# Performance work log

Measured on AMD Instinct MI355X. Metric: run time of the kernel, lower is better.

## Reference

```python
import jax, jax.numpy as jnp
import numpy as np

EPS = 1e-5
NEG_INF = -1e38


def q_shift(x, H, W, gamma=0.25, s=1):
    # x: (B, T, C) with T = H*W. Four channel groups shifted by 1 pixel in +W,-W,+H,-H.
    B, T, C = x.shape
    g = int(C * gamma)
    x4 = x.reshape(B, H, W, C)
    o0 = jnp.pad(x4[..., 0:g], ((0, 0), (0, 0), (s, 0), (0, 0)))[:, :, :W, :]      # shift right along W
    o1 = jnp.pad(x4[..., g:2 * g], ((0, 0), (0, 0), (0, s), (0, 0)))[:, :, s:, :]  # shift left along W
    o2 = jnp.pad(x4[..., 2 * g:3 * g], ((0, 0), (s, 0), (0, 0), (0, 0)))[:, :H, :, :]  # shift down along H
    o3 = jnp.pad(x4[..., 3 * g:4 * g], ((0, 0), (0, s), (0, 0), (0, 0)))[:, s:, :, :]  # shift up along H
    parts = [o0, o1, o2, o3]
    if 4 * g < C:
        parts.append(jnp.zeros((B, H, W, C - 4 * g), x.dtype))
    return jnp.concatenate(parts, axis=-1).reshape(B, T, C)


def wkv(w, u, k, v):
    # Numerically-stable RWKV WKV recurrence.
    # w,u: (C,); k,v: (B,T,C) -> y: (B,T,C)
    B, T, C = k.shape

    def step(carry, kv):
        a, b, p = carry
        kt, vt = kv
        ww = u + kt
        p2 = jnp.maximum(p, ww)
        e1 = jnp.exp(p - p2)
        e2 = jnp.exp(ww - p2)
        y = (e1 * a + e2 * vt) / (e1 * b + e2)
        ww2 = p + w
        p3 = jnp.maximum(ww2, kt)
        f1 = jnp.exp(ww2 - p3)
        f2 = jnp.exp(kt - p3)
        return (f1 * a + f2 * vt, f1 * b + f2, p3), y

    init = (jnp.zeros((B, C), k.dtype), jnp.zeros((B, C), k.dtype),
            jnp.full((B, C), NEG_INF, k.dtype))
    kT = jnp.swapaxes(k, 0, 1)
    vT = jnp.swapaxes(v, 0, 1)
    _, ys = jax.lax.scan(step, init, (kT, vT))
    return jnp.swapaxes(ys, 0, 1)


def layer_norm(x, g, b):
    m = jnp.mean(x, axis=-1, keepdims=True)
    v = jnp.mean(jnp.square(x - m), axis=-1, keepdims=True)
    return (x - m) * jax.lax.rsqrt(v + EPS) * g + b


def setup_inputs() -> dict:
    key = jax.random.key(0)
    ks = jax.random.split(key, 16)
    B, H, W, C = 8, 64, 64, 768
    T = H * W
    sc = 1.0 / np.sqrt(C)
    inp = {
        "x": jax.random.normal(ks[0], (B, T, C), jnp.float32),
        "spatial_decay": jax.random.normal(ks[1], (C,), jnp.float32) * 0.1,
        "spatial_first": jax.random.normal(ks[2], (C,), jnp.float32) * 0.1,
        "mix_k": jax.random.uniform(ks[3], (1, 1, C), jnp.float32),
        "mix_v": jax.random.uniform(ks[4], (1, 1, C), jnp.float32),
        "mix_r": jax.random.uniform(ks[5], (1, 1, C), jnp.float32),
        "Wk": jax.random.normal(ks[6], (C, C), jnp.float32) * sc,
        "Wv": jax.random.normal(ks[7], (C, C), jnp.float32) * sc,
        "Wr": jax.random.normal(ks[8], (C, C), jnp.float32) * sc,
        "Wo": jax.random.normal(ks[9], (C, C), jnp.float32) * sc,
        "ln_g": jnp.ones((C,), jnp.float32),
        "ln_b": jnp.zeros((C,), jnp.float32),
        "Wd1": jax.random.normal(ks[10], (C, C // 4), jnp.float32) * sc,
        "bd1": jnp.zeros((C // 4,), jnp.float32),
        "Wd2": jax.random.normal(ks[11], (C // 4, C), jnp.float32) * (2.0 / np.sqrt(C)),
        "bd2": jnp.full((C,), -3.0, jnp.float32),
        "H": H,
        "W": W,
    }
    return inp


def reference(x, spatial_decay, spatial_first, mix_k, mix_v, mix_r,
              Wk, Wv, Wr, Wo, ln_g, ln_b, Wd1, bd1, Wd2, bd2, H, W):
    B, T, C = x.shape
    xx = q_shift(x, H, W)
    xk = x * mix_k + xx * (1.0 - mix_k)
    xv = x * mix_v + xx * (1.0 - mix_v)
    xr = x * mix_r + xx * (1.0 - mix_r)
    k = xk @ Wk
    v = xv @ Wv
    sr = jax.nn.sigmoid(xr @ Wr)
    # frequency-adaptive decay modulation from global context
    gctx = jnp.mean(x, axis=1)                       # (B, C)
    h = jnp.tanh(gctx @ Wd1 + bd1)                   # (B, C/4)
    mod = jax.nn.sigmoid(h @ Wd2 + bd2)              # (B, C)
    w = spatial_decay + jnp.mean(mod, axis=0)        # (C,)
    y = wkv(w, spatial_first, k, v)                  # (B, T, C)
    y = layer_norm(y, ln_g, ln_b)
    return (sr * y) @ Wo
```

## Files before the change

kernel.cpp:

```cpp
#include <hip/hip_runtime.h>
#include <hip/hip_bf16.h>

typedef __hip_bfloat16 bf16;
typedef short short8 __attribute__((ext_vector_type(8)));
typedef float f32x4 __attribute__((ext_vector_type(4)));

#define T_SEQ 4096
#define HH 64
#define WW2 64
#define C_DIM 768
#define CQ 192
#define LCH 32
#define NCH (T_SEQ / LCH)
#define NCG (C_DIM / 8)

__device__ __forceinline__ float b2f(bf16 h) { return __bfloat162float(h); }
__device__ __forceinline__ bf16 f2b(float f) { return __float2bfloat16(f); }
__device__ __forceinline__ float sigmoid_stable(float m) {
  float e = __expf(-fabsf(m));
  return (m >= 0.f) ? 1.f / (1.f + e) : e / (1.f + e);
}

union V16 { uint4 u; bf16 h[8]; };

__global__ void k_detect(const unsigned* __restrict__ p, int* __restrict__ flag) {
  if (threadIdx.x == 0 && blockIdx.x == 0)
    *flag = ((p[0] & 0xFFFFu) == 0u) ? 1 : 0;
}

__global__ void k_convert_b(const void* __restrict__ src, bf16* __restrict__ dst,
                            int n, const int* __restrict__ flag) {
  int i = blockIdx.x * blockDim.x + threadIdx.x;
  if (i >= n) return;
  dst[i] = (*flag) ? f2b(((const float*)src)[i]) : ((const bf16*)src)[i];
}

__global__ void k_convert_f(const void* __restrict__ src, float* __restrict__ dst,
                            int n, const int* __restrict__ flag) {
  int i = blockIdx.x * blockDim.x + threadIdx.x;
  if (i >= n) return;
  dst[i] = (*flag) ? ((const float*)src)[i] : b2f(((const bf16*)src)[i]);
}

__global__ void k_transpose_d(const void* __restrict__ src, bf16* __restrict__ dst,
                              const int* __restrict__ flag) {
  __shared__ bf16 tile[32][33];
  bool f32 = (*flag != 0);
  int bx = blockIdx.x * 32, by = blockIdx.y * 32;
  int tx = threadIdx.x, ty = threadIdx.y;
  for (int j = ty; j < 32; j += 8) {
    size_t idx = (size_t)(by + j) * C_DIM + bx + tx;
    tile[j][tx] = f32 ? f2b(((const float*)src)[idx]) : ((const bf16*)src)[idx];
  }
  __syncthreads();
  for (int j = ty; j < 32; j += 8)
    dst[(size_t)(bx + j) * C_DIM + by + tx] = tile[tx][j];
}

__global__ void k_shift_mix1(const void* __restrict__ xsrc,
                             const float* __restrict__ mix,
                             bf16* __restrict__ dst, int BT,
                             const int* __restrict__ flag) {
  int idx = blockIdx.x * blockDim.x + threadIdx.x;
  if (idx >= BT * (C_DIM / 8)) return;
  bool f32 = (*flag != 0);
  int c8 = (idx % (C_DIM / 8)) * 8;
  int tg = idx / (C_DIM / 8);
  int t = tg & (T_SEQ - 1);
  int hh = t >> 6, ww = t & (WW2 - 1);
  int g = c8 / CQ;
  int d; bool valid;
  if (g == 0)      { valid = (ww >= 1);        d = -1;   }
  else if (g == 1) { valid = (ww <= WW2 - 2);  d = 1;    }
  else if (g == 2) { valid = (hh >= 1);        d = -WW2; }
  else             { valid = (hh <= HH - 2);   d = WW2;  }
  ptrdiff_t base = (ptrdiff_t)tg * C_DIM + c8;
  float fx[8], fxx[8];
  if (f32) {
    const float* xp = (const float*)xsrc;
#pragma unroll
    for (int i = 0; i < 8; i++) fx[i] = xp[base + i];
    if (valid) {
#pragma unroll
      for (int i = 0; i < 8; i++) fxx[i] = xp[base + (ptrdiff_t)d * C_DIM + i];
    } else {
#pragma unroll
      for (int i = 0; i < 8; i++) fxx[i] = 0.f;
    }
  } else {
    const bf16* xp = (const bf16*)xsrc;
    V16 xin; xin.u = *(const uint4*)(xp + base);
    V16 xxv;
    if (valid) xxv.u = *(const uint4*)(xp + base + (ptrdiff_t)d * C_DIM);
    else       xxv.u = make_uint4(0u, 0u, 0u, 0u);
#pragma unroll
    for (int i = 0; i < 8; i++) { fx[i] = b2f(xin.h[i]); fxx[i] = b2f(xxv.h[i]); }
  }
  V16 o;
#pragma unroll
  for (int i = 0; i < 8; i++)
    o.h[i] = f2b(fxx[i] + mix[c8 + i] * (fx[i] - fxx[i]));
  *(uint4*)(dst + base) = o.u;
}

__global__ void k_gctx(const void* __restrict__ xsrc, float* __restrict__ gctx,
                       const int* __restrict__ flag) {
  bool f32 = (*flag != 0);
  int c = threadIdx.x;
  int chunk = blockIdx.x;
  int b = blockIdx.y;
  size_t base = ((size_t)b * T_SEQ + (size_t)chunk * 128) * C_DIM + c;
  float s = 0.f;
  if (f32) {
    const float* p = (const float*)xsrc;
    for (int t = 0; t < 128; t++) s += p[base + (size_t)t * C_DIM];
  } else {
    const bf16* p = (const bf16*)xsrc;
    for (int t = 0; t < 128; t++) s += b2f(p[base + (size_t)t * C_DIM]);
  }
  atomicAdd(&gctx[b * C_DIM + c], s);
}

__global__ void k_mod(const float* __restrict__ gctx,
                      const bf16* __restrict__ Wd1, const float* __restrict__ bd1,
                      const bf16* __restrict__ Wd2, const float* __restrict__ bd2,
                      float* __restrict__ wsum, int B) {
  __shared__ float hsh[CQ];
  int b = blockIdx.x, j = threadIdx.x;
  const float invT = 1.0f / (float)T_SEQ;
  float acc = bd1[j];
  for (int i = 0; i < C_DIM; i++)
    acc += (gctx[b * C_DIM + i] * invT) * b2f(Wd1[(size_t)i * CQ + j]);
  hsh[j] = tanhf(acc);
  __syncthreads();
  float invB = 1.0f / (float)B;
  for (int cc = j; cc < C_DIM; cc += CQ) {
    float m = bd2[cc];
    for (int jj = 0; jj < CQ; jj++)
      m += hsh[jj] * b2f(Wd2[(size_t)jj * C_DIM + cc]);
    atomicAdd(&wsum[cc], sigmoid_stable(m) * invB);
  }
}

__device__ __forceinline__ void g2l16(const void* g, void* s) {
  __builtin_amdgcn_global_load_lds(
      (const __attribute__((address_space(1))) unsigned int*)g,
      (__attribute__((address_space(3))) unsigned int*)s, 16, 0, 0);
}

template <int MODE>
__global__ __launch_bounds__(256) void k_gemm_bt(const bf16* __restrict__ A,
                                                 const bf16* __restrict__ Bt,
                                                 void* __restrict__ Cout,
                                                 const int* __restrict__ flag) {
  const int K = C_DIM, N = C_DIM;
  __shared__ bf16 sA[128 * 32];
  __shared__ bf16 sB[128 * 32];
  int tid = threadIdx.x;
  int wv = tid >> 6, lane = tid & 63;
  int lm = lane & 15, quad = lane >> 4;
  int m0 = blockIdx.x * 128, n0 = blockIdx.y * 128;
  int wm = (wv & 1) * 64, wn = (wv >> 1) * 64;
  bool f32out = (MODE == 2) && (*flag != 0);

  f32x4 acc[4][4];
#pragma unroll
  for (int i = 0; i < 4; i++)
#pragma unroll
    for (int j = 0; j < 4; j++) acc[i][j] = f32x4{0.f, 0.f, 0.f, 0.f};

  const bf16* Abase = A + (size_t)m0 * K;
  const bf16* Bbase = Bt + (size_t)n0 * K;
  int ci0 = wv * 128 + lane;
  int ci1 = wv * 128 + 64 + lane;

  for (int kc = 0; kc < K; kc += 32) {
    g2l16(Abase + (size_t)(ci0 >> 2) * K + kc + (ci0 & 3) * 8, (char*)sA + (size_t)(wv * 128) * 16);
    g2l16(Abase + (size_t)(ci1 >> 2) * K + kc + (ci1 & 3) * 8, (char*)sA + (size_t)(wv * 128 + 64) * 16);
    g2l16(Bbase + (size_t)(ci0 >> 2) * K + kc + (ci0 & 3) * 8, (char*)sB + (size_t)(wv * 128) * 16);
    g2l16(Bbase + (size_t)(ci1 >> 2) * K + kc + (ci1 & 3) * 8, (char*)sB + (size_t)(wv * 128 + 64) * 16);
    __syncthreads();
    short8 af[4], bfr[4];
#pragma unroll
    for (int i = 0; i < 4; i++)
      af[i] = *(const short8*)(sA + (size_t)(wm + i * 16 + lm) * 32 + quad * 8);
#pragma unroll
    for (int j = 0; j < 4; j++)
      bfr[j] = *(const short8*)(sB + (size_t)(wn + j * 16 + lm) * 32 + quad * 8);
#pragma unroll
    for (int i = 0; i < 4; i++)
#pragma unroll
      for (int j = 0; j < 4; j++)
        acc[i][j] = __builtin_amdgcn_mfma_f32_16x16x32_bf16(af[i], bfr[j], acc[i][j], 0, 0, 0);
    __syncthreads();
  }
#pragma unroll
  for (int i = 0; i < 4; i++)
#pragma unroll
    for (int j = 0; j < 4; j++)
#pragma unroll
      for (int r = 0; r < 4; r++) {
        int m = wm + i * 16 + quad * 4 + r;
        int n = wn + j * 16 + lm;
        float v = acc[i][j][r];
        if (MODE == 1) v = sigmoid_stable(v);
        size_t oidx = (size_t)(m0 + m) * N + n0 + n;
        if (MODE == 2) {
          if (f32out) ((float*)Cout)[oidx] = v;
          else        ((bf16*)Cout)[oidx] = f2b(v);
        } else {
          ((bf16*)Cout)[oidx] = f2b(v);
        }
      }
}


__global__ __launch_bounds__(256) void k_wkv_p1(
    const bf16* __restrict__ kb, const bf16* __restrict__ vb,
    const float* __restrict__ sd, const float* __restrict__ wsum,
    float* __restrict__ ca, float* __restrict__ cb, float* __restrict__ cp, int B) {
  int gid = blockIdx.x * 256 + threadIdx.x;
  if (gid >= B * NCH * NCG) return;
  int cg = gid % NCG;
  int ch = (gid / NCG) % NCH;
  int b  = gid / (NCG * NCH);
  int c0 = cg * 8;
  float w[8], a[8], bb[8], p[8];
#pragma unroll
  for (int i = 0; i < 8; i++) {
    w[i] = sd[c0 + i] + wsum[c0 + i];
    a[i] = 0.f; bb[i] = 0.f; p[i] = -1e38f;
  }
  const bf16* kp = kb + ((size_t)b * T_SEQ + (size_t)ch * LCH) * C_DIM + c0;
  const bf16* vp = vb + ((size_t)b * T_SEQ + (size_t)ch * LCH) * C_DIM + c0;
  V16 kv, vv, kn, vn;
  kv.u = *(const uint4*)kp;
  vv.u = *(const uint4*)vp;
  kn = kv; vn = vv;
  for (int t = 0; t < LCH; t++) {
    if (t + 1 < LCH) {
      kn.u = *(const uint4*)(kp + (size_t)(t + 1) * C_DIM);
      vn.u = *(const uint4*)(vp + (size_t)(t + 1) * C_DIM);
    }
#pragma unroll
    for (int i = 0; i < 8; i++) {
      float kt = b2f(kv.h[i]), vt = b2f(vv.h[i]);
      float ww2 = p[i] + w[i];
      float p3 = fmaxf(ww2, kt);
      float f1 = __expf(ww2 - p3);
      float f2 = __expf(kt - p3);
      a[i] = f1 * a[i] + f2 * vt;
      bb[i] = f1 * bb[i] + f2;
      p[i] = p3;
    }
    kv = kn; vv = vn;
  }
  size_t so = ((size_t)b * NCH + ch) * C_DIM + c0;
#pragma unroll
  for (int i = 0; i < 8; i++) { ca[so + i] = a[i]; cb[so + i] = bb[i]; cp[so + i] = p[i]; }
}

__global__ void k_wkv_p2(float* __restrict__ ca, float* __restrict__ cb,
                         float* __restrict__ cp,
                         const float* __restrict__ sd, const float* __restrict__ wsum,
                         int B) {
  int tid = blockIdx.x * blockDim.x + threadIdx.x;
  if (tid >= B * C_DIM) return;
  int b = tid / C_DIM, c = tid % C_DIM;
  float wL = (sd[c] + wsum[c]) * (float)LCH;
  float a = 0.f, bb = 0.f, p = -1e38f;
  for (int base = 0; base < NCH; base += 16) {
    float la[16], lb[16], lp[16];
#pragma unroll
    for (int j = 0; j < 16; j++) {
      size_t idx = ((size_t)b * NCH + base + j) * C_DIM + c;
      la[j] = ca[idx]; lb[j] = cb[idx]; lp[j] = cp[idx];
    }
#pragma unroll
    for (int j = 0; j < 16; j++) {
      size_t idx = ((size_t)b * NCH + base + j) * C_DIM + c;
      ca[idx] = a; cb[idx] = bb; cp[idx] = p;
      float pw = p + wL;
      float pn = fmaxf(pw, lp[j]);
      float e1 = __expf(pw - pn);
      float e2 = __expf(lp[j] - pn);
      a = e1 * a + e2 * la[j];
      bb = e1 * bb + e2 * lb[j];
      p = pn;
    }
  }
}

__global__ __launch_bounds__(256) void k_wkv_p3(
    const bf16* __restrict__ kb, const bf16* __restrict__ vb,
    const float* __restrict__ sd, const float* __restrict__ sf,
    const float* __restrict__ wsum,
    const float* __restrict__ ca, const float* __restrict__ cb,
    const float* __restrict__ cp, bf16* __restrict__ y, int B) {
  int gid = blockIdx.x * 256 + threadIdx.x;
  if (gid >= B * NCH * NCG) return;
  int cg = gid % NCG;
  int ch = (gid / NCG) % NCH;
  int b  = gid / (NCG * NCH);
  int c0 = cg * 8;
  size_t so = ((size_t)b * NCH + ch) * C_DIM + c0;
  float w[8], u[8], aa[8], bb[8], pp[8];
#pragma unroll
  for (int i = 0; i < 8; i++) {
    w[i] = sd[c0 + i] + wsum[c0 + i];
    u[i] = sf[c0 + i];
    aa[i] = ca[so + i]; bb[i] = cb[so + i]; pp[i] = cp[so + i];
  }
  const bf16* kp = kb + ((size_t)b * T_SEQ + (size_t)ch * LCH) * C_DIM + c0;
  const bf16* vp = vb + ((size_t)b * T_SEQ + (size_t)ch * LCH) * C_DIM + c0;
  bf16* yp = y + ((size_t)b * T_SEQ + (size_t)ch * LCH) * C_DIM + c0;
  V16 kv, vv, kn, vn;
  kv.u = *(const uint4*)kp;
  vv.u = *(const uint4*)vp;
  kn = kv; vn = vv;
  for (int t = 0; t < LCH; t++) {
    if (t + 1 < LCH) {
      kn.u = *(const uint4*)(kp + (size_t)(t + 1) * C_DIM);
      vn.u = *(const uint4*)(vp + (size_t)(t + 1) * C_DIM);
    }
    V16 o;
#pragma unroll
    for (int i = 0; i < 8; i++) {
      float kt = b2f(kv.h[i]), vt = b2f(vv.h[i]);
      float ww = u[i] + kt;
      float p2 = fmaxf(pp[i], ww);
      float e1 = __expf(pp[i] - p2);
      float e2 = __expf(ww - p2);
      o.h[i] = f2b((e1 * aa[i] + e2 * vt) / (e1 * bb[i] + e2));
      float ww2 = pp[i] + w[i];
      float p3 = fmaxf(ww2, kt);
      float f1 = __expf(ww2 - p3);
      float f2 = __expf(kt - p3);
      aa[i] = f1 * aa[i] + f2 * vt;
      bb[i] = f1 * bb[i] + f2;
      pp[i] = p3;
    }
    *(uint4*)(yp + (size_t)t * C_DIM) = o.u;
    kv = kn; vv = vn;
  }
}

__global__ __launch_bounds__(256) void k_ln_mul(const bf16* __restrict__ y,
                                                const bf16* __restrict__ sr,
                                                const float* __restrict__ lng,
                                                const float* __restrict__ lnb,
                                                bf16* __restrict__ out) {
  int row = blockIdx.x;
  int tid = threadIdx.x;
  const bf16* yr = y + (size_t)row * C_DIM;
  float v0 = b2f(yr[tid]), v1 = b2f(yr[tid + 256]), v2 = b2f(yr[tid + 512]);
  float s1 = v0 + v1 + v2;
  float s2 = v0 * v0 + v1 * v1 + v2 * v2;
#pragma unroll
  for (int off = 32; off >= 1; off >>= 1) {
    s1 += __shfl_xor(s1, off, 64);
    s2 += __shfl_xor(s2, off, 64);
  }
  __shared__ float sh1[4], sh2[4];
  int wv = tid >> 6, lane = tid & 63;
  if (lane == 0) { sh1[wv] = s1; sh2[wv] = s2; }
  __syncthreads();
  float t1 = sh1[0] + sh1[1] + sh1[2] + sh1[3];
  float t2 = sh2[0] + sh2[1] + sh2[2] + sh2[3];
  float mean = t1 * (1.f / (float)C_DIM);
  float var = t2 * (1.f / (float)C_DIM) - mean * mean;
  float rstd = rsqrtf(var + 1e-5f);
  const bf16* srr = sr + (size_t)row * C_DIM;
  bf16* orow = out + (size_t)row * C_DIM;
  float vv[3] = {v0, v1, v2};
#pragma unroll
  for (int kk = 0; kk < 3; kk++) {
    int c = tid + kk * 256;
    float r = (vv[kk] - mean) * rstd * lng[c] + lnb[c];
    orow[c] = f2b(r * b2f(srr[c]));
  }
}

extern "C" void kernel_launch(void* const* d_in, const int* in_sizes, int n_in,
                              void* d_out, int out_size, void* d_ws, size_t ws_size,
                              hipStream_t stream) {
  const void* x   = d_in[0];
  const void* sd  = d_in[1];
  const void* sf  = d_in[2];
  const void* mk  = d_in[3];
  const void* mv  = d_in[4];
  const void* mr  = d_in[5];
  const void* Wk  = d_in[6];
  const void* Wv  = d_in[7];
  const void* Wr  = d_in[8];
  const void* Wo  = d_in[9];
  const void* lng = d_in[10];
  const void* lnb = d_in[11];
  const void* Wd1 = d_in[12];
  const void* bd1 = d_in[13];
  const void* Wd2 = d_in[14];
  const void* bd2 = d_in[15];

  const int C = in_sizes[1];
  const int BT = in_sizes[0] / C;
  const int B = BT / T_SEQ;

  char* ws = (char*)d_ws;
  const size_t S = (size_t)BT * C * sizeof(bf16);
  const size_t WB = (size_t)C * C * sizeof(bf16);
  const size_t WD = (size_t)C * CQ * sizeof(bf16);
  bf16* slot0 = (bf16*)(ws + 0 * S);
  bf16* slot1 = (bf16*)(ws + 1 * S);
  char* p = ws + 2 * S;
  bf16* WkT = (bf16*)p; p += WB;
  bf16* WvT = (bf16*)p; p += WB;
  bf16* WrT = (bf16*)p; p += WB;
  bf16* WoT = (bf16*)p; p += WB;
  bf16* Wd1c = (bf16*)p; p += WD;
  bf16* Wd2c = (bf16*)p; p += WD;
  float* sd_f  = (float*)p; p += C * 4;
  float* sf_f  = (float*)p; p += C * 4;
  float* mk_f  = (float*)p; p += C * 4;
  float* mv_f  = (float*)p; p += C * 4;
  float* mr_f  = (float*)p; p += C * 4;
  float* lng_f = (float*)p; p += C * 4;
  float* lnb_f = (float*)p; p += C * 4;
  float* bd2_f = (float*)p; p += C * 4;
  float* bd1_f = (float*)p; p += CQ * 4;
  float* gctx  = (float*)p; p += (size_t)B * C * 4;
  float* wsum  = (float*)p; p += C * 4;
  int* flag    = (int*)p; p += 16;
  p = (char*)(((uintptr_t)p + 15) & ~(uintptr_t)15);
  float* ca = (float*)p; p += (size_t)B * NCH * C * 4;
  float* cb = (float*)p; p += (size_t)B * NCH * C * 4;
  float* cp = (float*)p; p += (size_t)B * NCH * C * 4;

  bf16* stage = (bf16*)d_out;

  k_detect<<<1, 64, 0, stream>>>((const unsigned*)lng, flag);
  hipMemsetAsync(gctx, 0, (size_t)(B * C + C) * sizeof(float), stream);

  k_convert_f<<<3, 256, 0, stream>>>(sd,  sd_f,  C, flag);
  k_convert_f<<<3, 256, 0, stream>>>(sf,  sf_f,  C, flag);
  k_convert_f<<<3, 256, 0, stream>>>(mk,  mk_f,  C, flag);
  k_convert_f<<<3, 256, 0, stream>>>(mv,  mv_f,  C, flag);
  k_convert_f<<<3, 256, 0, stream>>>(mr,  mr_f,  C, flag);
  k_convert_f<<<3, 256, 0, stream>>>(lng, lng_f, C, flag);
  k_convert_f<<<3, 256, 0, stream>>>(lnb, lnb_f, C, flag);
  k_convert_f<<<3, 256, 0, stream>>>(bd2, bd2_f, C, flag);
  k_convert_f<<<1, 256, 0, stream>>>(bd1, bd1_f, CQ, flag);
  k_convert_b<<<(C * CQ + 255) / 256, 256, 0, stream>>>(Wd1, Wd1c, C * CQ, flag);
  k_convert_b<<<(C * CQ + 255) / 256, 256, 0, stream>>>(Wd2, Wd2c, C * CQ, flag);

  dim3 tb(32, 8), tg(C / 32, C / 32);
  k_transpose_d<<<tg, tb, 0, stream>>>(Wk, WkT, flag);
  k_transpose_d<<<tg, tb, 0, stream>>>(Wv, WvT, flag);
  k_transpose_d<<<tg, tb, 0, stream>>>(Wr, WrT, flag);
  k_transpose_d<<<tg, tb, 0, stream>>>(Wo, WoT, flag);

  k_gctx<<<dim3(32, B), C, 0, stream>>>(x, gctx, flag);
  k_mod<<<B, CQ, 0, stream>>>(gctx, Wd1c, bd1_f, Wd2c, bd2_f, wsum, B);

  int nthr = BT * (C / 8);
  int nblk = (nthr + 255) / 256;
  dim3 gg(BT / 128, C / 128);

  k_shift_mix1<<<nblk, 256, 0, stream>>>(x, mk_f, stage, BT, flag);
  k_gemm_bt<0><<<gg, 256, 0, stream>>>(stage, WkT, slot0, flag);
  k_shift_mix1<<<nblk, 256, 0, stream>>>(x, mv_f, stage, BT, flag);
  k_gemm_bt<0><<<gg, 256, 0, stream>>>(stage, WvT, slot1, flag);

  int scan_threads = B * NCH * NCG;
  k_wkv_p1<<<(scan_threads + 255) / 256, 256, 0, stream>>>(slot0, slot1, sd_f, wsum, ca, cb, cp, B);
  k_wkv_p2<<<(B * C + 255) / 256, 256, 0, stream>>>(ca, cb, cp, sd_f, wsum, B);
  k_wkv_p3<<<(scan_threads + 255) / 256, 256, 0, stream>>>(slot0, slot1, sd_f, sf_f, wsum, ca, cb, cp, stage, B);

  k_shift_mix1<<<nblk, 256, 0, stream>>>(x, mr_f, slot0, BT, flag);
  k_gemm_bt<1><<<gg, 256, 0, stream>>>(slot0, WrT, slot1, flag);
  k_ln_mul<<<BT, 256, 0, stream>>>(stage, slot1, lng_f, lnb_f, slot0);
  k_gemm_bt<2><<<gg, 256, 0, stream>>>(slot0, WoT, d_out, flag);
}
```

Before: 716.4 us.

## Fuse shift-mix passes, fold LayerNorm into gemm epilogue, and stage stores via LDS

The three shift-mix passes are merged into one kernel that reads x once, writes xk/xv/xr, and also emits per-block partial sums for the global context, so the separate gctx pass goes away. The LayerNorm-multiply kernel is split into a row-stats kernel plus an epilogue in the Wr gemm that applies sigmoid, normalization and the multiply. Gemm output now goes through LDS for coalesced 16-byte stores, with a float path for f32 output. The grid is swapped so blocks along N are adjacent. The scan loops are unrolled four deep with prefetching, and the small parameter conversions are batched into one launch. The fused path needs an extra full-size workspace slot and falls back to the old order when the workspace is too small.

```diff
diff --git a/kernel.cpp b/kernel.cpp
--- a/kernel.cpp
+++ b/kernel.cpp
@@ -13,6 +13,7 @@
 #define LCH 32
 #define NCH (T_SEQ / LCH)
 #define NCG (C_DIM / 8)
+#define TCH 16
 
 __device__ __forceinline__ float b2f(bf16 h) { return __bfloat162float(h); }
 __device__ __forceinline__ bf16 f2b(float f) { return __float2bfloat16(f); }
@@ -35,11 +36,20 @@
   dst[i] = (*flag) ? f2b(((const float*)src)[i]) : ((const bf16*)src)[i];
 }
 
-__global__ void k_convert_f(const void* __restrict__ src, float* __restrict__ dst,
-                            int n, const int* __restrict__ flag) {
-  int i = blockIdx.x * blockDim.x + threadIdx.x;
-  if (i >= n) return;
-  dst[i] = (*flag) ? ((const float*)src)[i] : b2f(((const bf16*)src)[i]);
+__global__ void k_convert_small(
+    const void* s0, const void* s1, const void* s2, const void* s3, const void* s4,
+    const void* s5, const void* s6, const void* s7, const void* s8,
+    float* d0, float* d1, float* d2, float* d3, float* d4,
+    float* d5, float* d6, float* d7, float* d8, const int* __restrict__ flag) {
+  const void* srcs[9] = {s0, s1, s2, s3, s4, s5, s6, s7, s8};
+  float* dsts[9] = {d0, d1, d2, d3, d4, d5, d6, d7, d8};
+  int a = blockIdx.x;
+  int n = (a == 8) ? CQ : C_DIM;
+  const void* s = srcs[a];
+  float* d = dsts[a];
+  bool f32 = (*flag != 0);
+  for (int i = threadIdx.x; i < n; i += 256)
+    d[i] = f32 ? ((const float*)s)[i] : b2f(((const bf16*)s)[i]);
 }
 
 __global__ void k_transpose_d(const void* __restrict__ src, bf16* __restrict__ dst,
@@ -103,6 +113,93 @@
   *(uint4*)(dst + base) = o.u;
 }
 
+__global__ __launch_bounds__(256) void k_shift_mix3(
+    const void* __restrict__ xsrc,
+    const float* __restrict__ mk, const float* __restrict__ mv, const float* __restrict__ mr,
+    bf16* __restrict__ xk, bf16* __restrict__ xv, bf16* __restrict__ xr,
+    float* __restrict__ gpart, const int* __restrict__ flag) {
+  __shared__ float sh[C_DIM];
+  int tid = threadIdx.x;
+  sh[tid] = 0.f; sh[tid + 256] = 0.f; sh[tid + 512] = 0.f;
+  __syncthreads();
+  int gid = blockIdx.x * 256 + tid;
+  bool f32 = (*flag != 0);
+  int cg = gid % NCG;
+  int tc = gid / NCG;
+  int c0 = cg * 8;
+  int b = tc / (T_SEQ / TCH);
+  int t0 = (tc % (T_SEQ / TCH)) * TCH;
+  int g = c0 / CQ;
+  float mkv[8], mvv[8], mrv[8];
+#pragma unroll
+  for (int i = 0; i < 8; i++) { mkv[i] = mk[c0 + i]; mvv[i] = mv[c0 + i]; mrv[i] = mr[c0 + i]; }
+  float gs[8];
+#pragma unroll
+  for (int i = 0; i < 8; i++) gs[i] = 0.f;
+  for (int tt = 0; tt < TCH; tt++) {
+    int t = t0 + tt;
+    int hh = t >> 6, ww = t & (WW2 - 1);
+    int d; bool valid;
+    if (g == 0)      { valid = (ww >= 1);        d = -1;   }
+    else if (g == 1) { valid = (ww <= WW2 - 2);  d = 1;    }
+    else if (g == 2) { valid = (hh >= 1);        d = -WW2; }
+    else             { valid = (hh <= HH - 2);   d = WW2;  }
+    ptrdiff_t base = ((ptrdiff_t)b * T_SEQ + t) * C_DIM + c0;
+    float fx[8], fxx[8];
+    if (f32) {
+      const float* xp = (const float*)xsrc;
+      float4 a0 = *(const float4*)(xp + base);
+      float4 a1 = *(const float4*)(xp + base + 4);
+      fx[0] = a0.x; fx[1] = a0.y; fx[2] = a0.z; fx[3] = a0.w;
+      fx[4] = a1.x; fx[5] = a1.y; fx[6] = a1.z; fx[7] = a1.w;
+      if (valid) {
+        float4 b0 = *(const float4*)(xp + base + (ptrdiff_t)d * C_DIM);
+        float4 b1 = *(const float4*)(xp + base + (ptrdiff_t)d * C_DIM + 4);
+        fxx[0] = b0.x; fxx[1] = b0.y; fxx[2] = b0.z; fxx[3] = b0.w;
+        fxx[4] = b1.x; fxx[5] = b1.y; fxx[6] = b1.z; fxx[7] = b1.w;
+      } else {
+#pragma unroll
+        for (int i = 0; i < 8; i++) fxx[i] = 0.f;
+      }
+    } else {
+      const bf16* xp = (const bf16*)xsrc;
+      V16 xin; xin.u = *(const uint4*)(xp + base);
+      V16 xxv;
+      if (valid) xxv.u = *(const uint4*)(xp + base + (ptrdiff_t)d * C_DIM);
+      else       xxv.u = make_uint4(0u, 0u, 0u, 0u);
+#pragma unroll
+      for (int i = 0; i < 8; i++) { fx[i] = b2f(xin.h[i]); fxx[i] = b2f(xxv.h[i]); }
+    }
+    V16 ok, ov, orr;
+#pragma unroll
+    for (int i = 0; i < 8; i++) {
+      gs[i] += fx[i];
+      ok.h[i]  = f2b(fxx[i] + mkv[i] * (fx[i] - fxx[i]));
+      ov.h[i]  = f2b(fxx[i] + mvv[i] * (fx[i] - fxx[i]));
+      orr.h[i] = f2b(fxx[i] + mrv[i] * (fx[i] - fxx[i]));
+    }
+    *(uint4*)(xk + base) = ok.u;
+    *(uint4*)(xv + base) = ov.u;
+    *(uint4*)(xr + base) = orr.u;
+  }
+#pragma unroll
+  for (int i = 0; i < 8; i++) atomicAdd(&sh[c0 + i], gs[i]);
+  __syncthreads();
+  float* gp = gpart + (size_t)blockIdx.x * C_DIM;
+  gp[tid] = sh[tid]; gp[tid + 256] = sh[tid + 256]; gp[tid + 512] = sh[tid + 512];
+}
+
+__global__ void k_gctx_reduce(const float* __restrict__ gpart, float* __restrict__ gctx,
+                              int B, int blk_per_b) {
+  int idx = blockIdx.x * 256 + threadIdx.x;
+  if (idx >= B * C_DIM) return;
+  int b = idx / C_DIM, c = idx % C_DIM;
+  const float* pp = gpart + (size_t)b * blk_per_b * C_DIM + c;
+  float s = 0.f;
+  for (int j = 0; j < blk_per_b; j++) s += pp[(size_t)j * C_DIM];
+  gctx[idx] = s;
+}
+
 __global__ void k_gctx(const void* __restrict__ xsrc, float* __restrict__ gctx,
                        const int* __restrict__ flag) {
   bool f32 = (*flag != 0);
@@ -149,19 +246,20 @@
 }
 
 template <int MODE>
-__global__ __launch_bounds__(256) void k_gemm_bt(const bf16* __restrict__ A,
-                                                 const bf16* __restrict__ Bt,
-                                                 void* __restrict__ Cout,
-                                                 const int* __restrict__ flag) {
+__global__ __launch_bounds__(256) void k_gemm_bt(
+    const bf16* __restrict__ A, const bf16* __restrict__ Bt, void* __restrict__ Cout,
+    const bf16* __restrict__ Y, const float* __restrict__ stats,
+    const float* __restrict__ lng, const float* __restrict__ lnb,
+    const int* __restrict__ flag) {
   const int K = C_DIM, N = C_DIM;
-  __shared__ bf16 sA[128 * 32];
-  __shared__ bf16 sB[128 * 32];
+  __shared__ __align__(16) char smem[32768];
+  bf16* sA = (bf16*)smem;
+  bf16* sB = (bf16*)(smem + 8192);
   int tid = threadIdx.x;
   int wv = tid >> 6, lane = tid & 63;
   int lm = lane & 15, quad = lane >> 4;
-  int m0 = blockIdx.x * 128, n0 = blockIdx.y * 128;
+  int n0 = blockIdx.x * 128, m0 = blockIdx.y * 128;
   int wm = (wv & 1) * 64, wn = (wv >> 1) * 64;
-  bool f32out = (MODE == 2) && (*flag != 0);
 
   f32x4 acc[4][4];
 #pragma unroll
@@ -194,26 +292,107 @@
         acc[i][j] = __builtin_amdgcn_mfma_f32_16x16x32_bf16(af[i], bfr[j], acc[i][j], 0, 0, 0);
     __syncthreads();
   }
-#pragma unroll
-  for (int i = 0; i < 4; i++)
-#pragma unroll
-    for (int j = 0; j < 4; j++)
-#pragma unroll
-      for (int r = 0; r < 4; r++) {
-        int m = wm + i * 16 + quad * 4 + r;
-        int n = wn + j * 16 + lm;
-        float v = acc[i][j][r];
-        if (MODE == 1) v = sigmoid_stable(v);
-        size_t oidx = (size_t)(m0 + m) * N + n0 + n;
-        if (MODE == 2) {
-          if (f32out) ((float*)Cout)[oidx] = v;
-          else        ((bf16*)Cout)[oidx] = f2b(v);
-        } else {
-          ((bf16*)Cout)[oidx] = f2b(v);
+
+  bool f32out = (MODE == 2) && (*flag != 0);
+  if (!f32out) {
+    bf16* sC = (bf16*)smem;
+#pragma unroll
+    for (int i = 0; i < 4; i++)
+#pragma unroll
+      for (int j = 0; j < 4; j++)
+#pragma unroll
+        for (int r = 0; r < 4; r++) {
+          int m = wm + i * 16 + quad * 4 + r;
+          int n = wn + j * 16 + lm;
+          float v = acc[i][j][r];
+          if (MODE == 1 || MODE == 3) v = sigmoid_stable(v);
+          sC[m * 128 + n] = f2b(v);
         }
+    __syncthreads();
+    int c16 = tid & 15, r0 = tid >> 4;
+#pragma unroll
+    for (int it = 0; it < 8; it++) {
+      int r = r0 + it * 16;
+      V16 val; val.u = *(const uint4*)(sC + r * 128 + c16 * 8);
+      size_t gbase = (size_t)(m0 + r) * N + n0 + c16 * 8;
+      if (MODE == 3) {
+        float mu = stats[2 * (m0 + r)], rs = stats[2 * (m0 + r) + 1];
+        V16 yv; yv.u = *(const uint4*)(Y + gbase);
+        const float* lg = lng + n0 + c16 * 8;
+        const float* lb = lnb + n0 + c16 * 8;
+        V16 o;
+#pragma unroll
+        for (int jj = 0; jj < 8; jj++)
+          o.h[jj] = f2b(b2f(val.h[jj]) * ((b2f(yv.h[jj]) - mu) * rs * lg[jj] + lb[jj]));
+        *(uint4*)((bf16*)Cout + gbase) = o.u;
+      } else {
+        *(uint4*)((bf16*)Cout + gbase) = val.u;
       }
-}
-
+    }
+  } else {
+    float* sCf = (float*)smem;
+#pragma unroll
+    for (int half = 0; half < 2; half++) {
+      if (half) __syncthreads();
+      if ((wv & 1) == half) {
+#pragma unroll
+        for (int i = 0; i < 4; i++)
+#pragma unroll
+          for (int j = 0; j < 4; j++)
+#pragma unroll
+            for (int r = 0; r < 4; r++) {
+              int mrow = i * 16 + quad * 4 + r;
+              int n = wn + j * 16 + lm;
+              sCf[mrow * 128 + n] = acc[i][j][r];
+            }
+      }
+      __syncthreads();
+      int c32 = tid & 31, r0 = tid >> 5;
+#pragma unroll
+      for (int it = 0; it < 8; it++) {
+        int r = r0 + it * 8;
+        float4 val = *(const float4*)(sCf + r * 128 + c32 * 4);
+        *(float4*)((float*)Cout + (size_t)(m0 + half * 64 + r) * N + n0 + c32 * 4) = val;
+      }
+    }
+  }
+}
+
+__device__ __forceinline__ void wkv_acc_step(const V16& kv, const V16& vv,
+    const float* __restrict__ w, float* a, float* bb, float* p) {
+#pragma unroll
+  for (int i = 0; i < 8; i++) {
+    float kt = b2f(kv.h[i]), vt = b2f(vv.h[i]);
+    float ww2 = p[i] + w[i];
+    float p3 = fmaxf(ww2, kt);
+    float f1 = __expf(ww2 - p3);
+    float f2 = __expf(kt - p3);
+    a[i] = f1 * a[i] + f2 * vt;
+    bb[i] = f1 * bb[i] + f2;
+    p[i] = p3;
+  }
+}
+
+__device__ __forceinline__ void wkv_out_step(const V16& kv, const V16& vv,
+    const float* __restrict__ w, const float* __restrict__ u,
+    float* aa, float* bb, float* pp, V16& o) {
+#pragma unroll
+  for (int i = 0; i < 8; i++) {
+    float kt = b2f(kv.h[i]), vt = b2f(vv.h[i]);
+    float ww = u[i] + kt;
+    float p2 = fmaxf(pp[i], ww);
+    float e1 = __expf(pp[i] - p2);
+    float e2 = __expf(ww - p2);
+    o.h[i] = f2b((e1 * aa[i] + e2 * vt) / (e1 * bb[i] + e2));
+    float ww2 = pp[i] + w[i];
+    float p3 = fmaxf(ww2, kt);
+    float f1 = __expf(ww2 - p3);
+    float f2 = __expf(kt - p3);
+    aa[i] = f1 * aa[i] + f2 * vt;
+    bb[i] = f1 * bb[i] + f2;
+    pp[i] = p3;
+  }
+}
 
 __global__ __launch_bounds__(256) void k_wkv_p1(
     const bf16* __restrict__ kb, const bf16* __restrict__ vb,
@@ -225,39 +404,36 @@
   int ch = (gid / NCG) % NCH;
   int b  = gid / (NCG * NCH);
   int c0 = cg * 8;
-  float w[8], a[8], bb[8], p[8];
+  float w[8], a[8], bbv[8], p[8];
 #pragma unroll
   for (int i = 0; i < 8; i++) {
     w[i] = sd[c0 + i] + wsum[c0 + i];
-    a[i] = 0.f; bb[i] = 0.f; p[i] = -1e38f;
+    a[i] = 0.f; bbv[i] = 0.f; p[i] = -1e38f;
   }
   const bf16* kp = kb + ((size_t)b * T_SEQ + (size_t)ch * LCH) * C_DIM + c0;
   const bf16* vp = vb + ((size_t)b * T_SEQ + (size_t)ch * LCH) * C_DIM + c0;
-  V16 kv, vv, kn, vn;
-  kv.u = *(const uint4*)kp;
-  vv.u = *(const uint4*)vp;
-  kn = kv; vn = vv;
-  for (int t = 0; t < LCH; t++) {
-    if (t + 1 < LCH) {
-      kn.u = *(const uint4*)(kp + (size_t)(t + 1) * C_DIM);
-      vn.u = *(const uint4*)(vp + (size_t)(t + 1) * C_DIM);
-    }
-#pragma unroll
-    for (int i = 0; i < 8; i++) {
-      float kt = b2f(kv.h[i]), vt = b2f(vv.h[i]);
-      float ww2 = p[i] + w[i];
-      float p3 = fmaxf(ww2, kt);
-      float f1 = __expf(ww2 - p3);
-      float f2 = __expf(kt - p3);
-      a[i] = f1 * a[i] + f2 * vt;
-      bb[i] = f1 * bb[i] + f2;
-      p[i] = p3;
-    }
-    kv = kn; vv = vn;
-  }
+  V16 k0, k1, k2, k3, v0, v1, v2, v3;
+  k0.u = *(const uint4*)(kp);              v0.u = *(const uint4*)(vp);
+  k1.u = *(const uint4*)(kp + C_DIM);      v1.u = *(const uint4*)(vp + C_DIM);
+  k2.u = *(const uint4*)(kp + 2 * C_DIM);  v2.u = *(const uint4*)(vp + 2 * C_DIM);
+  k3.u = *(const uint4*)(kp + 3 * C_DIM);  v3.u = *(const uint4*)(vp + 3 * C_DIM);
+  for (int t = 0; t + 4 < LCH; t += 4) {
+    wkv_acc_step(k0, v0, w, a, bbv, p);
+    k0.u = *(const uint4*)(kp + (size_t)(t + 4) * C_DIM); v0.u = *(const uint4*)(vp + (size_t)(t + 4) * C_DIM);
+    wkv_acc_step(k1, v1, w, a, bbv, p);
+    k1.u = *(const uint4*)(kp + (size_t)(t + 5) * C_DIM); v1.u = *(const uint4*)(vp + (size_t)(t + 5) * C_DIM);
+    wkv_acc_step(k2, v2, w, a, bbv, p);
+    k2.u = *(const uint4*)(kp + (size_t)(t + 6) * C_DIM); v2.u = *(const uint4*)(vp + (size_t)(t + 6) * C_DIM);
+    wkv_acc_step(k3, v3, w, a, bbv, p);
+    k3.u = *(const uint4*)(kp + (size_t)(t + 7) * C_DIM); v3.u = *(const uint4*)(vp + (size_t)(t + 7) * C_DIM);
+  }
+  wkv_acc_step(k0, v0, w, a, bbv, p);
+  wkv_acc_step(k1, v1, w, a, bbv, p);
+  wkv_acc_step(k2, v2, w, a, bbv, p);
+  wkv_acc_step(k3, v3, w, a, bbv, p);
   size_t so = ((size_t)b * NCH + ch) * C_DIM + c0;
 #pragma unroll
-  for (int i = 0; i < 8; i++) { ca[so + i] = a[i]; cb[so + i] = bb[i]; cp[so + i] = p[i]; }
+  for (int i = 0; i < 8; i++) { ca[so + i] = a[i]; cb[so + i] = bbv[i]; cp[so + i] = p[i]; }
 }
 
 __global__ void k_wkv_p2(float* __restrict__ ca, float* __restrict__ cb,
@@ -304,52 +480,47 @@
   int b  = gid / (NCG * NCH);
   int c0 = cg * 8;
   size_t so = ((size_t)b * NCH + ch) * C_DIM + c0;
-  float w[8], u[8], aa[8], bb[8], pp[8];
+  float w[8], u[8], aa[8], bbv[8], pp[8];
 #pragma unroll
   for (int i = 0; i < 8; i++) {
     w[i] = sd[c0 + i] + wsum[c0 + i];
     u[i] = sf[c0 + i];
-    aa[i] = ca[so + i]; bb[i] = cb[so + i]; pp[i] = cp[so + i];
+    aa[i] = ca[so + i]; bbv[i] = cb[so + i]; pp[i] = cp[so + i];
   }
   const bf16* kp = kb + ((size_t)b * T_SEQ + (size_t)ch * LCH) * C_DIM + c0;
   const bf16* vp = vb + ((size_t)b * T_SEQ + (size_t)ch * LCH) * C_DIM + c0;
   bf16* yp = y + ((size_t)b * T_SEQ + (size_t)ch * LCH) * C_DIM + c0;
-  V16 kv, vv, kn, vn;
-  kv.u = *(const uint4*)kp;
-  vv.u = *(const uint4*)vp;
-  kn = kv; vn = vv;
-  for (int t = 0; t < LCH; t++) {
-    if (t + 1 < LCH) {
-      kn.u = *(const uint4*)(kp + (size_t)(t + 1) * C_DIM);
-      vn.u = *(const uint4*)(vp + (size_t)(t + 1) * C_DIM);
-    }
-    V16 o;
-#pragma unroll
-    for (int i = 0; i < 8; i++) {
-      float kt = b2f(kv.h[i]), vt = b2f(vv.h[i]);
-      float ww = u[i] + kt;
-      float p2 = fmaxf(pp[i], ww);
-      float e1 = __expf(pp[i] - p2);
-      float e2 = __expf(ww - p2);
-      o.h[i] = f2b((e1 * aa[i] + e2 * vt) / (e1 * bb[i] + e2));
-      float ww2 = pp[i] + w[i];
-      float p3 = fmaxf(ww2, kt);
-      float f1 = __expf(ww2 - p3);
-      float f2 = __expf(kt - p3);
-      aa[i] = f1 * aa[i] + f2 * vt;
-      bb[i] = f1 * bb[i] + f2;
-      pp[i] = p3;
-    }
+  V16 k0, k1, k2, k3, v0, v1, v2, v3, o;
+  k0.u = *(const uint4*)(kp);              v0.u = *(const uint4*)(vp);
+  k1.u = *(const uint4*)(kp + C_DIM);      v1.u = *(const uint4*)(vp + C_DIM);
+  k2.u = *(const uint4*)(kp + 2 * C_DIM);  v2.u = *(const uint4*)(vp + 2 * C_DIM);
+  k3.u = *(const uint4*)(kp + 3 * C_DIM);  v3.u = *(const uint4*)(vp + 3 * C_DIM);
+  for (int t = 0; t + 4 < LCH; t += 4) {
+    wkv_out_step(k0, v0, w, u, aa, bbv, pp, o);
     *(uint4*)(yp + (size_t)t * C_DIM) = o.u;
-    kv = kn; vv = vn;
-  }
-}
-
-__global__ __launch_bounds__(256) void k_ln_mul(const bf16* __restrict__ y,
-                                                const bf16* __restrict__ sr,
-                                                const float* __restrict__ lng,
-                                                const float* __restrict__ lnb,
-                                                bf16* __restrict__ out) {
+    k0.u = *(const uint4*)(kp + (size_t)(t + 4) * C_DIM); v0.u = *(const uint4*)(vp + (size_t)(t + 4) * C_DIM);
+    wkv_out_step(k1, v1, w, u, aa, bbv, pp, o);
+    *(uint4*)(yp + (size_t)(t + 1) * C_DIM) = o.u;
+    k1.u = *(const uint4*)(kp + (size_t)(t + 5) * C_DIM); v1.u = *(const uint4*)(vp + (size_t)(t + 5) * C_DIM);
+    wkv_out_step(k2, v2, w, u, aa, bbv, pp, o);
+    *(uint4*)(yp + (size_t)(t + 2) * C_DIM) = o.u;
+    k2.u = *(const uint4*)(kp + (size_t)(t + 6) * C_DIM); v2.u = *(const uint4*)(vp + (size_t)(t + 6) * C_DIM);
+    wkv_out_step(k3, v3, w, u, aa, bbv, pp, o);
+    *(uint4*)(yp + (size_t)(t + 3) * C_DIM) = o.u;
+    k3.u = *(const uint4*)(kp + (size_t)(t + 7) * C_DIM); v3.u = *(const uint4*)(vp + (size_t)(t + 7) * C_DIM);
+  }
+  wkv_out_step(k0, v0, w, u, aa, bbv, pp, o);
+  *(uint4*)(yp + (size_t)(LCH - 4) * C_DIM) = o.u;
+  wkv_out_step(k1, v1, w, u, aa, bbv, pp, o);
+  *(uint4*)(yp + (size_t)(LCH - 3) * C_DIM) = o.u;
+  wkv_out_step(k2, v2, w, u, aa, bbv, pp, o);
+  *(uint4*)(yp + (size_t)(LCH - 2) * C_DIM) = o.u;
+  wkv_out_step(k3, v3, w, u, aa, bbv, pp, o);
+  *(uint4*)(yp + (size_t)(LCH - 1) * C_DIM) = o.u;
+}
+
+__global__ __launch_bounds__(256) void k_ln_stats(const bf16* __restrict__ y,
+                                                  float* __restrict__ stats) {
   int row = blockIdx.x;
   int tid = threadIdx.x;
   const bf16* yr = y + (size_t)row * C_DIM;
@@ -365,19 +536,13 @@
   int wv = tid >> 6, lane = tid & 63;
   if (lane == 0) { sh1[wv] = s1; sh2[wv] = s2; }
   __syncthreads();
-  float t1 = sh1[0] + sh1[1] + sh1[2] + sh1[3];
-  float t2 = sh2[0] + sh2[1] + sh2[2] + sh2[3];
-  float mean = t1 * (1.f / (float)C_DIM);
-  float var = t2 * (1.f / (float)C_DIM) - mean * mean;
-  float rstd = rsqrtf(var + 1e-5f);
-  const bf16* srr = sr + (size_t)row * C_DIM;
-  bf16* orow = out + (size_t)row * C_DIM;
-  float vv[3] = {v0, v1, v2};
-#pragma unroll
-  for (int kk = 0; kk < 3; kk++) {
-    int c = tid + kk * 256;
-    float r = (vv[kk] - mean) * rstd * lng[c] + lnb[c];
-    orow[c] = f2b(r * b2f(srr[c]));
+  if (tid == 0) {
+    float t1 = sh1[0] + sh1[1] + sh1[2] + sh1[3];
+    float t2 = sh2[0] + sh2[1] + sh2[2] + sh2[3];
+    float mean = t1 * (1.f / (float)C_DIM);
+    float var = t2 * (1.f / (float)C_DIM) - mean * mean;
+    stats[2 * row] = mean;
+    stats[2 * row + 1] = rsqrtf(var + 1e-5f);
   }
 }
 
@@ -405,13 +570,22 @@
   const int BT = in_sizes[0] / C;
   const int B = BT / T_SEQ;
 
-  char* ws = (char*)d_ws;
-  const size_t S = (size_t)BT * C * sizeof(bf16);
+  const size_t S  = (size_t)BT * C * sizeof(bf16);
   const size_t WB = (size_t)C * C * sizeof(bf16);
   const size_t WD = (size_t)C * CQ * sizeof(bf16);
-  bf16* slot0 = (bf16*)(ws + 0 * S);
-  bf16* slot1 = (bf16*)(ws + 1 * S);
-  char* p = ws + 2 * S;
+  const size_t CS = (size_t)B * NCH * C * sizeof(float);
+  const int nblk_mix = (BT / TCH) * NCG / 256;
+  const int blk_per_b = nblk_mix / B;
+  const size_t GP = (size_t)nblk_mix * C * sizeof(float);
+  const size_t rest = 4 * WB + 2 * WD + ((size_t)8 * C + CQ + (size_t)B * C + C) * 4
+                      + 16 + 15 + 3 * CS + (size_t)BT * 8 + GP + 256;
+  const bool fused = (ws_size >= 3 * S + rest);
+
+  char* p = (char*)d_ws;
+  bf16* slot0 = (bf16*)p; p += S;
+  bf16* slot1 = (bf16*)p; p += S;
+  bf16* slot2 = nullptr;
+  if (fused) { slot2 = (bf16*)p; p += S; }
   bf16* WkT = (bf16*)p; p += WB;
   bf16* WvT = (bf16*)p; p += WB;
   bf16* WrT = (bf16*)p; p += WB;
@@ -431,24 +605,20 @@
   float* wsum  = (float*)p; p += C * 4;
   int* flag    = (int*)p; p += 16;
   p = (char*)(((uintptr_t)p + 15) & ~(uintptr_t)15);
-  float* ca = (float*)p; p += (size_t)B * NCH * C * 4;
-  float* cb = (float*)p; p += (size_t)B * NCH * C * 4;
-  float* cp = (float*)p; p += (size_t)B * NCH * C * 4;
+  float* ca = (float*)p; p += CS;
+  float* cb = (float*)p; p += CS;
+  float* cp = (float*)p; p += CS;
+  float* stats = (float*)p; p += (size_t)BT * 8;
+  float* gpart = (float*)p; p += GP;
 
   bf16* stage = (bf16*)d_out;
 
   k_detect<<<1, 64, 0, stream>>>((const unsigned*)lng, flag);
   hipMemsetAsync(gctx, 0, (size_t)(B * C + C) * sizeof(float), stream);
 
-  k_convert_f<<<3, 256, 0, stream>>>(sd,  sd_f,  C, flag);
-  k_convert_f<<<3, 256, 0, stream>>>(sf,  sf_f,  C, flag);
-  k_convert_f<<<3, 256, 0, stream>>>(mk,  mk_f,  C, flag);
-  k_convert_f<<<3, 256, 0, stream>>>(mv,  mv_f,  C, flag);
-  k_convert_f<<<3, 256, 0, stream>>>(mr,  mr_f,  C, flag);
-  k_convert_f<<<3, 256, 0, stream>>>(lng, lng_f, C, flag);
-  k_convert_f<<<3, 256, 0, stream>>>(lnb, lnb_f, C, flag);
-  k_convert_f<<<3, 256, 0, stream>>>(bd2, bd2_f, C, flag);
-  k_convert_f<<<1, 256, 0, stream>>>(bd1, bd1_f, CQ, flag);
+  k_convert_small<<<9, 256, 0, stream>>>(sd, sf, mk, mv, mr, lng, lnb, bd2, bd1,
+                                         sd_f, sf_f, mk_f, mv_f, mr_f, lng_f, lnb_f,
+                                         bd2_f, bd1_f, flag);
   k_convert_b<<<(C * CQ + 255) / 256, 256, 0, stream>>>(Wd1, Wd1c, C * CQ, flag);
   k_convert_b<<<(C * CQ + 255) / 256, 256, 0, stream>>>(Wd2, Wd2c, C * CQ, flag);
 
@@ -458,25 +628,44 @@
   k_transpose_d<<<tg, tb, 0, stream>>>(Wr, WrT, flag);
   k_transpose_d<<<tg, tb, 0, stream>>>(Wo, WoT, flag);
 
-  k_gctx<<<dim3(32, B), C, 0, stream>>>(x, gctx, flag);
-  k_mod<<<B, CQ, 0, stream>>>(gctx, Wd1c, bd1_f, Wd2c, bd2_f, wsum, B);
-
-  int nthr = BT * (C / 8);
-  int nblk = (nthr + 255) / 256;
-  dim3 gg(BT / 128, C / 128);
-
-  k_shift_mix1<<<nblk, 256, 0, stream>>>(x, mk_f, stage, BT, flag);
-  k_gemm_bt<0><<<gg, 256, 0, stream>>>(stage, WkT, slot0, flag);
-  k_shift_mix1<<<nblk, 256, 0, stream>>>(x, mv_f, stage, BT, flag);
-  k_gemm_bt<0><<<gg, 256, 0, stream>>>(stage, WvT, slot1, flag);
-
+  dim3 gg(C / 128, BT / 128);
   int scan_threads = B * NCH * NCG;
-  k_wkv_p1<<<(scan_threads + 255) / 256, 256, 0, stream>>>(slot0, slot1, sd_f, wsum, ca, cb, cp, B);
-  k_wkv_p2<<<(B * C + 255) / 256, 256, 0, stream>>>(ca, cb, cp, sd_f, wsum, B);
-  k_wkv_p3<<<(scan_threads + 255) / 256, 256, 0, stream>>>(slot0, slot1, sd_f, sf_f, wsum, ca, cb, cp, stage, B);
-
-  k_shift_mix1<<<nblk, 256, 0, stream>>>(x, mr_f, slot0, BT, flag);
-  k_gemm_bt<1><<<gg, 256, 0, stream>>>(slot0, WrT, slot1, flag);
-  k_ln_mul<<<BT, 256, 0, stream>>>(stage, slot1, lng_f, lnb_f, slot0);
-  k_gemm_bt<2><<<gg, 256, 0, stream>>>(slot0, WoT, d_out, flag);
-}
+  int scan_blocks = (scan_threads + 255) / 256;
+
+  if (fused) {
+    k_shift_mix3<<<nblk_mix, 256, 0, stream>>>(x, mk_f, mv_f, mr_f,
+                                               slot0, stage, slot1, gpart, flag);
+    k_gctx_reduce<<<(B * C + 255) / 256, 256, 0, stream>>>(gpart, gctx, B, blk_per_b);
+    k_mod<<<B, CQ, 0, stream>>>(gctx, Wd1c, bd1_f, Wd2c, bd2_f, wsum, B);
+
+    k_gemm_bt<0><<<gg, 256, 0, stream>>>(slot0, WkT, slot2, nullptr, nullptr, nullptr, nullptr, flag);
+    k_gemm_bt<0><<<gg, 256, 0, stream>>>(stage, WvT, slot0, nullptr, nullptr, nullptr, nullptr, flag);
+
+    k_wkv_p1<<<scan_blocks, 256, 0, stream>>>(slot2, slot0, sd_f, wsum, ca, cb, cp, B);
+    k_wkv_p2<<<(B * C + 255) / 256, 256, 0, stream>>>(ca, cb, cp, sd_f, wsum, B);
+    k_wkv_p3<<<scan_blocks, 256, 0, stream>>>(slot2, slot0, sd_f, sf_f, wsum, ca, cb, cp, stage, B);
+
+    k_ln_stats<<<BT, 256, 0, stream>>>(stage, stats);
+    k_gemm_bt<3><<<gg, 256, 0, stream>>>(slot1, WrT, slot0, stage, stats, lng_f, lnb_f, flag);
+    k_gemm_bt<2><<<gg, 256, 0, stream>>>(slot0, WoT, d_out, nullptr, nullptr, nullptr, nullptr, flag);
+  } else {
+    int nthr = BT * (C / 8);
+    int nblk = (nthr + 255) / 256;
+    k_gctx<<<dim3(32, B), C, 0, stream>>>(x, gctx, flag);
+    k_mod<<<B, CQ, 0, stream>>>(gctx, Wd1c, bd1_f, Wd2c, bd2_f, wsum, B);
+
+    k_shift_mix1<<<nblk, 256, 0, stream>>>(x, mk_f, stage, BT, flag);
+    k_gemm_bt<0><<<gg, 256, 0, stream>>>(stage, WkT, slot0, nullptr, nullptr, nullptr, nullptr, flag);
+    k_shift_mix1<<<nblk, 256, 0, stream>>>(x, mv_f, stage, BT, flag);
+    k_gemm_bt<0><<<gg, 256, 0, stream>>>(stage, WvT, slot1, nullptr, nullptr, nullptr, nullptr, flag);
+
+    k_wkv_p1<<<scan_blocks, 256, 0, stream>>>(slot0, slot1, sd_f, wsum, ca, cb, cp, B);
+    k_wkv_p2<<<(B * C + 255) / 256, 256, 0, stream>>>(ca, cb, cp, sd_f, wsum, B);
+    k_wkv_p3<<<scan_blocks, 256, 0, stream>>>(slot0, slot1, sd_f, sf_f, wsum, ca, cb, cp, stage, B);
+
+    k_ln_stats<<<BT, 256, 0, stream>>>(stage, stats);
+    k_shift_mix1<<<nblk, 256, 0, stream>>>(x, mr_f, slot0, BT, flag);
+    k_gemm_bt<3><<<gg, 256, 0, stream>>>(slot0, WrT, slot1, stage, stats, lng_f, lnb_f, flag);
+    k_gemm_bt<2><<<gg, 256, 0, stream>>>(slot1, WoT, d_out, nullptr, nullptr, nullptr, nullptr, flag);
+  }
+}
```

Result: no change. 707.9 us (-1.2%).
